# Performance work log

Hardware: AMD Instinct MI355X
Metric: run time of the kernel (lower is better)

## Reference

```python
import jax, jax.numpy as jnp
import numpy as np

B, LK, D, H = 16, 4096, 1024, 16
DK = D // H
EPS = 1e-5
NEG = -1.0e9


def _layernorm(x, g, b):
    m = jnp.mean(x, axis=-1, keepdims=True)
    v = jnp.mean((x - m) ** 2, axis=-1, keepdims=True)
    return (x - m) * jax.lax.rsqrt(v + EPS) * g + b


def setup_inputs() -> dict:
    key0 = jax.random.key(0)
    ks = jax.random.split(key0, 12)

    def lin(k, fan_in, fan_out):
        # torch nn.Linear default-ish scale; stored as [in, out] so y = x @ W + b
        return jax.random.normal(k, (fan_in, fan_out), jnp.float32) / np.float32(np.sqrt(fan_in))

    return {
        "query": jax.random.normal(ks[0], (B, 1, D), jnp.float32),
        "key": jax.random.normal(ks[1], (B, LK, D), jnp.float32),
        "mask": jax.random.randint(ks[2], (B, 1, LK), 0, 2, jnp.int32),
        "Wq": lin(ks[3], D, D), "bq": jnp.zeros((D,), jnp.float32),
        "Wk": lin(ks[4], D, D), "bk": jnp.zeros((D,), jnp.float32),
        "Wv": lin(ks[5], D, D), "bv": jnp.zeros((D,), jnp.float32),
        "Wo": lin(ks[6], D, D), "bo": jnp.zeros((D,), jnp.float32),
        "raw_thr": jnp.full((H, 1, 1), 0.1, jnp.float32),
        "Wvp": lin(ks[7], 2 * D, D),  # v_proj, no bias
        "W1": lin(ks[8], D, 2 * D), "b1": jnp.zeros((2 * D,), jnp.float32),
        "W2": lin(ks[9], 2 * D, D), "b2": jnp.zeros((D,), jnp.float32),
        "g1": jnp.ones((D,), jnp.float32), "be1": jnp.zeros((D,), jnp.float32),
        "g2": jnp.ones((D,), jnp.float32), "be2": jnp.zeros((D,), jnp.float32),
    }


def reference(query, key, mask, Wq, bq, Wk, bk, Wv, bv, Wo, bo, raw_thr,
              Wvp, W1, b1, W2, b2, g1, be1, g2, be2):
    b = query.shape[0]
    lk = key.shape[1]
    # v = cat(key, query.repeat(1, Lk, 1)) @ Wvp   (query has seq_len 1)
    v_in = jnp.concatenate([key, jnp.broadcast_to(query, (b, lk, D))], axis=2)
    v = v_in @ Wvp  # [B, Lk, D]

    Q = (query @ Wq + bq).reshape(b, 1, H, DK).transpose(0, 2, 1, 3)   # [B,H,1,DK]
    K = (key @ Wk + bk).reshape(b, lk, H, DK).transpose(0, 2, 1, 3)    # [B,H,Lk,DK]
    V = (v @ Wv + bv).reshape(b, lk, H, DK).transpose(0, 2, 1, 3)      # [B,H,Lk,DK]

    scores = jnp.einsum("bhqd,bhkd->bhqk", Q, K) / jnp.sqrt(jnp.float32(DK))
    # padding mask: [B,1,Lk] -> [B,1,1,Lk]
    scores = jnp.where(mask[:, None] == 0, NEG, scores)
    # learned per-head threshold: softplus(raw_thr) -> [1,H,1,1]
    thr = jax.nn.softplus(raw_thr)[None]
    scores = jnp.where(scores <= thr, NEG, scores)
    attn = jax.nn.softmax(scores, axis=-1)

    x = jnp.einsum("bhqk,bhkd->bhqd", attn, V)            # [B,H,1,DK]
    x = x.transpose(0, 2, 1, 3).reshape(b, 1, H * DK)      # [B,1,D]
    attn_out = x @ Wo + bo

    x = _layernorm(query + attn_out, g1, be1)
    ff = jax.nn.relu(x @ W1 + b1) @ W2 + b2
    x = _layernorm(x + ff, g2, be2)
    return x
```

## Files before the change

### kernel.cpp

```cpp
#include <hip/hip_runtime.h>
#include <hip/hip_bf16.h>

#define NB 16
#define NHD 16
#define ND 1024
#define NLK 4096
#define NFF 2048

typedef float f32x4 __attribute__((ext_vector_type(4)));
typedef float f32x2 __attribute__((ext_vector_type(2)));
typedef __bf16 bf16x2v __attribute__((ext_vector_type(2)));
typedef __bf16 bf16x4v __attribute__((ext_vector_type(4)));
typedef __bf16 bf16x8 __attribute__((ext_vector_type(8)));

__global__ void k_fill(float* out, int n, float v) {
  int i = blockIdx.x * 256 + threadIdx.x;
  if (i < n) out[i] = v;
}

__device__ __forceinline__ void gbar(unsigned* ctr, unsigned* flg, unsigned nblk) {
  __syncthreads();
  if (threadIdx.x == 0) {
    __hip_atomic_fetch_add(ctr, 1u, __ATOMIC_RELEASE, __HIP_MEMORY_SCOPE_AGENT);
    if (blockIdx.x == 0) {
      while (__hip_atomic_load(ctr, __ATOMIC_RELAXED, __HIP_MEMORY_SCOPE_AGENT) < nblk)
        __builtin_amdgcn_s_sleep(8);
      __hip_atomic_store(flg, 1u, __ATOMIC_RELEASE, __HIP_MEMORY_SCOPE_AGENT);
    } else {
      while (__hip_atomic_load(flg, __ATOMIC_RELAXED, __HIP_MEMORY_SCOPE_AGENT) == 0)
        __builtin_amdgcn_s_sleep(8);
    }
    __builtin_amdgcn_fence(__ATOMIC_ACQUIRE, "agent");
  }
  __syncthreads();
}

__global__ __launch_bounds__(256) void k_pre(const float* __restrict__ Wq,
                                             const float* __restrict__ bq,
                                             const float* __restrict__ Wvp,
                                             const float* __restrict__ query,
                                             const float* __restrict__ Wk,
                                             const float* __restrict__ bk,
                                             float* __restrict__ Qrow,
                                             float* __restrict__ cvec,
                                             __hip_bfloat16* __restrict__ wvpt,
                                             __hip_bfloat16* __restrict__ t_bf,
                                             float* __restrict__ s0,
                                             unsigned* __restrict__ bar) {
  __shared__ float pmem[9472];
  int blk = blockIdx.x;
  int t = threadIdx.x;
  if (blk < 128) {
    int which = blk >> 6;
    int jb = blk & 3;
    int i0 = ((blk >> 2) & 15) * 64;
    int j = jb * 256 + t;
    {
      int e = t * 4;
      int b = e >> 6, ii = e & 63;
      float4 v = *(const float4*)(query + (size_t)b * ND + i0 + ii);
      pmem[ii * 20 + b] = v.x;
      pmem[(ii + 1) * 20 + b] = v.y;
      pmem[(ii + 2) * 20 + b] = v.z;
      pmem[(ii + 3) * 20 + b] = v.w;
    }
    __syncthreads();
    float acc[16];
#pragma unroll
    for (int q = 0; q < 16; ++q) acc[q] = 0.f;
    for (int ii = 0; ii < 64; ++ii) {
      int i = i0 + ii;
      float wv = which ? Wvp[(size_t)(ND + i) * ND + j] : Wq[(size_t)i * ND + j];
      float qv[16];
      const float4* qp = (const float4*)&pmem[ii * 20];
      *(float4*)&qv[0] = qp[0];
      *(float4*)&qv[4] = qp[1];
      *(float4*)&qv[8] = qp[2];
      *(float4*)&qv[12] = qp[3];
#pragma unroll
      for (int q = 0; q < 16; ++q) acc[q] += wv * qv[q];
    }
    float* out = which ? cvec : Qrow;
    float bias = (!which && i0 == 0) ? bq[j] : 0.f;
#pragma unroll
    for (int q = 0; q < 16; ++q) atomicAdd(&out[q * ND + j], acc[q] + bias);
  } else {
    int tb = blk - 128;
    int n0 = (tb & 15) * 64;
    int k0base = (tb >> 4) * 256;
    for (int it = 0; it < 4; ++it) {
      int k0 = k0base + it * 64;
#pragma unroll
      for (int i = 0; i < 4; ++i) {
        int idx = t * 4 + i * 1024;
        int kk = idx >> 6, nn = idx & 63;
        float4 v = *(const float4*)(Wvp + (size_t)(k0 + kk) * ND + n0 + nn);
        pmem[kk * 68 + nn] = v.x;
        pmem[kk * 68 + nn + 1] = v.y;
        pmem[kk * 68 + nn + 2] = v.z;
        pmem[kk * 68 + nn + 3] = v.w;
      }
      __syncthreads();
#pragma unroll
      for (int i = 0; i < 4; ++i) {
        int idx = t * 4 + i * 1024;
        int nn = idx >> 6, kk = idx & 63;
        bf16x4v o;
#pragma unroll
        for (int j = 0; j < 4; ++j) o[j] = (__bf16)pmem[(kk + j) * 68 + nn];
        *(bf16x4v*)((__bf16*)wvpt + (size_t)(n0 + nn) * ND + k0 + kk) = o;
      }
      __syncthreads();
    }
  }
  gbar(&bar[5 * 32], &bar[256 + 5 * 32], 192);
  {
    int h = blk & 15, dblk = blk >> 4;
    float* qs = pmem;
    float* wks = pmem + 1024;
    if (blk < 128) {
      int lin = t * 4;
      int bb = lin >> 6, dk = lin & 63;
      *(float4*)&qs[bb * 64 + dk] = *(const float4*)(Qrow + bb * ND + h * 64 + dk);
#pragma unroll
      for (int e = 0; e < 8; ++e) {
        int l2 = e * 1024 + t * 4;
        int d = l2 >> 6, dk2 = l2 & 63;
        *(float4*)&wks[d * 66 + dk2] =
            *(const float4*)(Wk + (size_t)(dblk * 128 + d) * ND + h * 64 + dk2);
      }
    }
    __syncthreads();
    if (blk < 128) {
      if (dblk == 0 && t < 16) {
        float a = 0.f;
        const float* bkh = bk + h * 64;
        for (int jj = 0; jj < 64; ++jj) a += bkh[jj] * qs[t * 64 + jj];
        s0[t * 16 + h] = a;
      }
      int d = t >> 1, bh = (t & 1) * 8;
      float acc[8];
#pragma unroll
      for (int q = 0; q < 8; ++q) acc[q] = 0.f;
      for (int dk = 0; dk < 64; ++dk) {
        float wv = wks[d * 66 + dk];
#pragma unroll
        for (int q = 0; q < 8; ++q) acc[q] += wv * qs[(bh + q) * 64 + dk];
      }
#pragma unroll
      for (int q = 0; q < 8; ++q)
        t_bf[(size_t)((bh + q) * 16 + h) * ND + dblk * 128 + d] = (__hip_bfloat16)acc[q];
    }
  }
}

__global__ __launch_bounds__(512, 4) void k_flash(const float* __restrict__ key,
                                                  const __hip_bfloat16* __restrict__ t_bf,
                                                  const float* __restrict__ s0,
                                                  const float* __restrict__ raw_thr,
                                                  const int* __restrict__ mask,
                                                  __hip_bfloat16* __restrict__ pu,
                                                  float* __restrict__ mloc,
                                                  float* __restrict__ lloc) {
  int ch = blockIdx.x, b = blockIdx.y;
  int t = threadIdx.x;
  int wv = t >> 6, lane = t & 63, l15 = lane & 15, g4 = lane >> 4;
  __shared__ __align__(16) unsigned char lds_arena[79360];
  __bf16* kstage = (__bf16*)lds_arena;
  __bf16* psb = (__bf16*)(lds_arena + 65536);
  float* scr = (float*)(lds_arena + 74752);
  float* wls = (float*)(lds_arena + 76928);
  float* sm = (float*)(lds_arena + 78976);
  float* mrun = sm;
  float* lrun = sm + 16;
  float* fact = sm + 32;
  float* mnewv = sm + 48;
  float* thv = sm + 64;
  float* s0v = sm + 80;

  f32x2 pu_r[16];
#pragma unroll
  for (int h = 0; h < 16; ++h) pu_r[h] = (f32x2){0.f, 0.f};
  if (t < 16) {
    mrun[t] = -1.0e9f;
    lrun[t] = 0.f;
    thv[t] = log1pf(expf(raw_thr[t]));
    s0v[t] = s0[b * 16 + t];
  }
  __syncthreads();
  const float* keyb = key + (size_t)b * NLK * ND;
  const __hip_bfloat16* tb = t_bf + (size_t)(b * 16 + l15) * ND;
  int dsl = wv * 128;
  __bf16* kst_w = kstage + wv * 4096;
  int kk = t >> 4, hh = t & 15;
  int c16 = lane >> 2, bofs = (lane & 3) * 2;
  for (int sp = 0; sp < 4; ++sp) {
    int ks0 = ch * 128 + sp * 32;
    f32x4 sa0 = {0.f, 0.f, 0.f, 0.f}, sa1 = {0.f, 0.f, 0.f, 0.f};
#pragma unroll
    for (int st = 0; st < 4; ++st) {
      int d = dsl + st * 32 + g4 * 8;
      bf16x8 bfr = *(const bf16x8*)(tb + d);
      const float* a0p = keyb + (size_t)(ks0 + l15) * ND + d;
      const float* a1p = a0p + (size_t)16 * ND;
      float a0[8], a1[8];
      *(float4*)&a0[0] = *(const float4*)a0p;
      *(float4*)&a0[4] = *(const float4*)(a0p + 4);
      *(float4*)&a1[0] = *(const float4*)a1p;
      *(float4*)&a1[4] = *(const float4*)(a1p + 4);
      bf16x8 af0, af1;
#pragma unroll
      for (int j = 0; j < 8; ++j) {
        af0[j] = (__bf16)a0[j];
        af1[j] = (__bf16)a1[j];
      }
      int pos = (((st * 4 + g4) ^ l15) & 15) * 8;
      *(bf16x8*)(kst_w + l15 * 128 + pos) = af0;
      *(bf16x8*)(kst_w + (16 + l15) * 128 + pos) = af1;
      sa0 = __builtin_amdgcn_mfma_f32_16x16x32_bf16(af0, bfr, sa0, 0, 0, 0);
      sa1 = __builtin_amdgcn_mfma_f32_16x16x32_bf16(af1, bfr, sa1, 0, 0, 0);
    }
#pragma unroll
    for (int r = 0; r < 4; ++r) {
      psb[(wv * 32 + g4 * 4 + r) * 18 + l15] = (__bf16)sa0[r];
      psb[(wv * 32 + 16 + g4 * 4 + r) * 18 + l15] = (__bf16)sa1[r];
    }
    __syncthreads();
    float sum = 0.f;
#pragma unroll
    for (int w = 0; w < 8; ++w) sum += (float)psb[(w * 32 + kk) * 18 + hh];
    float sc_ = (sum + s0v[hh]) * 0.125f;
    int mv = mask[b * NLK + ks0 + kk];
    float sv = (mv != 0 && sc_ > thv[hh]) ? sc_ : -1.0e9f;
    scr[kk * 17 + hh] = sv;
    __syncthreads();
    if (wv == 0) {
      float m = -3.4e38f;
#pragma unroll
      for (int j = 0; j < 8; ++j) m = fmaxf(m, scr[(g4 * 8 + j) * 17 + l15]);
      m = fmaxf(m, __shfl_xor(m, 16, 64));
      m = fmaxf(m, __shfl_xor(m, 32, 64));
      if (lane < 16) {
        float mn = fmaxf(mrun[lane], m);
        mnewv[lane] = mn;
        fact[lane] = expf(mrun[lane] - mn);
        mrun[lane] = mn;
      }
    }
    __syncthreads();
    float w = expf(sv - mnewv[hh]);
    scr[kk * 17 + hh] = w;
    wls[kk * 16 + hh] = w;
    __syncthreads();
    if (wv == 0) {
      float s = 0.f;
#pragma unroll
      for (int j = 0; j < 8; ++j) s += scr[(g4 * 8 + j) * 17 + l15];
      s += __shfl_xor(s, 16, 64);
      s += __shfl_xor(s, 32, 64);
      if (lane < 16) lrun[lane] = lrun[lane] * fact[lane] + s;
    }
#pragma unroll
    for (int h = 0; h < 16; ++h) pu_r[h] *= fact[h];
    for (int k = 0; k < 32; ++k) {
      int phys = ((c16 ^ k) & 15) * 8;
      unsigned u = *(const unsigned*)(kst_w + k * 128 + phys + bofs);
      f32x2 kv;
      kv[0] = __uint_as_float(u << 16);
      kv[1] = __uint_as_float(u & 0xffff0000u);
      const f32x4* wr = (const f32x4*)&wls[k * 16];
      f32x4 w0 = wr[0], w1 = wr[1], w2 = wr[2], w3 = wr[3];
#pragma unroll
      for (int q = 0; q < 4; ++q) {
        pu_r[q] += w0[q] * kv;
        pu_r[4 + q] += w1[q] * kv;
        pu_r[8 + q] += w2[q] * kv;
        pu_r[12 + q] += w3[q] * kv;
      }
    }
  }
  int dlane = dsl + lane * 2;
  size_t pubase = (size_t)((b * 32 + ch) * 16) * ND + dlane;
#pragma unroll
  for (int h = 0; h < 16; ++h) {
    bf16x2v o;
    o[0] = (__bf16)pu_r[h][0];
    o[1] = (__bf16)pu_r[h][1];
    *(bf16x2v*)((__bf16*)pu + pubase + (size_t)h * ND) = o;
  }
  if (t < 16) {
    mloc[(b * 32 + ch) * 16 + t] = mrun[t];
    lloc[(b * 32 + ch) * 16 + t] = lrun[t];
  }
}

__global__ __launch_bounds__(256) void k_tail(
    const __hip_bfloat16* __restrict__ pu, const float* __restrict__ mloc,
    const float* __restrict__ lloc, __hip_bfloat16* __restrict__ u_bf,
    const __hip_bfloat16* __restrict__ wvpt,
    const float* __restrict__ cvec, const float* __restrict__ Wv,
    const float* __restrict__ bv, float* __restrict__ attn_x,
    const float* __restrict__ Wo, const float* __restrict__ bo,
    const float* __restrict__ query, float* __restrict__ r1,
    const float* __restrict__ g1, const float* __restrict__ be1,
    const float* __restrict__ W1, float* __restrict__ h1,
    const float* __restrict__ b1, const float* __restrict__ W2,
    float* __restrict__ out2, const float* __restrict__ b2,
    const float* __restrict__ g2, const float* __restrict__ be2,
    float* __restrict__ outp, unsigned* __restrict__ bar) {
  __shared__ float smf[2176];
  int blk = blockIdx.x, t = threadIdx.x;
  int wv = t >> 6, lane = t & 63, l15 = lane & 15, g4 = lane >> 4;

  {
    int g = blk * 256 + t;
    if (g < 16384) {
      attn_x[g] = 0.f;
      r1[g] = 0.f;
      out2[g] = 0.f;
    }
    if (g < 32768) h1[g] = 0.f;
    int b = blk >> 4, h = blk & 15;
    if (t < 32) {
      float m = mloc[(b * 32 + t) * 16 + h];
      float l = lloc[(b * 32 + t) * 16 + h];
      float mg = m;
      for (int o = 16; o > 0; o >>= 1) mg = fmaxf(mg, __shfl_xor(mg, o, 32));
      float term = l * expf(m - mg);
      float ls = term;
      for (int o = 16; o > 0; o >>= 1) ls += __shfl_xor(ls, o, 32);
      smf[t] = expf(m - mg) / ls;
    }
    __syncthreads();
    int d = t * 4;
    f32x4 acc = {0.f, 0.f, 0.f, 0.f};
    for (int c = 0; c < 32; ++c) {
      bf16x4v v4 = *(const bf16x4v*)((const __bf16*)pu +
                                     (size_t)((b * 32 + c) * 16 + h) * ND + d);
      f32x4 v = {(float)v4[0], (float)v4[1], (float)v4[2], (float)v4[3]};
      acc += smf[c] * v;
    }
    bf16x4v o;
#pragma unroll
    for (int j = 0; j < 4; ++j) o[j] = (__bf16)acc[j];
    *(bf16x4v*)((__bf16*)u_bf + (size_t)(b * 16 + h) * ND + d) = o;
  }
  gbar(&bar[0 * 32], &bar[256 + 0 * 32], 256);

  {
    int h = blk >> 4, d0 = (blk & 15) * 64;
    float* vb = smf;
    const __hip_bfloat16* ub = u_bf + (size_t)(l15 * 16 + h) * ND;
    const __hip_bfloat16* wb = wvpt + (size_t)(d0 + wv * 16 + l15) * ND;
    f32x4 acc = {0.f, 0.f, 0.f, 0.f};
    for (int ks = 0; ks < 32; ++ks) {
      int d = ks * 32 + g4 * 8;
      bf16x8 a = *(const bf16x8*)(ub + d);
      bf16x8 bb = *(const bf16x8*)(wb + d);
      acc = __builtin_amdgcn_mfma_f32_16x16x32_bf16(a, bb, acc, 0, 0, 0);
    }
#pragma unroll
    for (int r = 0; r < 4; ++r) {
      int b = g4 * 4 + r;
      int nn = wv * 16 + l15;
      vb[b * 68 + nn] = acc[r] + cvec[(size_t)b * ND + d0 + nn];
    }
    __syncthreads();
    int joff = t & 63, bg = t >> 6;
    int j = h * 64 + joff;
    float ax[4] = {0.f, 0.f, 0.f, 0.f};
    for (int dd = 0; dd < 64; ++dd) {
      float wv_ = Wv[(size_t)(d0 + dd) * ND + j];
#pragma unroll
      for (int q = 0; q < 4; ++q) ax[q] += wv_ * vb[(bg * 4 + q) * 68 + dd];
    }
#pragma unroll
    for (int q = 0; q < 4; ++q) {
      float val = ax[q];
      if ((blk & 15) == 0) val += bv[j];
      atomicAdd(&attn_x[(size_t)(bg * 4 + q) * ND + j], val);
    }
  }
  gbar(&bar[1 * 32], &bar[256 + 1 * 32], 256);

  if (blk < 128) {
    int j0 = (blk & 7) * 128;
    int d0 = (blk >> 3) * 64;
    float* ax = smf;
    {
      int lin = t * 4;
      int bb = lin >> 6, dd = lin & 63;
      *(float4*)&ax[bb * 68 + dd] = *(const float4*)(attn_x + (size_t)bb * ND + d0 + dd);
    }
    __syncthreads();
    int joff = t & 127, bg = t >> 7;
    int j = j0 + joff;
    float acc[8];
#pragma unroll
    for (int q = 0; q < 8; ++q) acc[q] = 0.f;
    for (int dd = 0; dd < 64; ++dd) {
      float wv_ = Wo[(size_t)(d0 + dd) * ND + j];
#pragma unroll
      for (int q = 0; q < 8; ++q) acc[q] += wv_ * ax[(bg * 8 + q) * 68 + dd];
    }
#pragma unroll
    for (int q = 0; q < 8; ++q) {
      int bb = bg * 8 + q;
      float val = acc[q];
      if ((blk >> 3) == 0) val += bo[j] + query[(size_t)bb * ND + j];
      atomicAdd(&r1[(size_t)bb * ND + j], val);
    }
  } else {
    __syncthreads();
  }
  gbar(&bar[2 * 32], &bar[256 + 2 * 32], 256);

  if (blk < 128) {
    int n = (blk & 7) * 256 + t;
    int d0 = (blk >> 3) * 64;
    float* xs = smf;
    float* mv_s = smf + 1984;
    float* iv_s = smf + 2000;
    {
      int row = t >> 4, seg = t & 15;
      float s = 0.f, s2 = 0.f;
      const float* rp = r1 + (size_t)row * ND + seg * 64;
      for (int q = 0; q < 16; ++q) {
        float4 v = *(const float4*)(rp + q * 4);
        s += v.x + v.y + v.z + v.w;
        s2 += v.x * v.x + v.y * v.y + v.z * v.z + v.w * v.w;
      }
      for (int o = 1; o < 16; o <<= 1) {
        s += __shfl_xor(s, o, 16);
        s2 += __shfl_xor(s2, o, 16);
      }
      if (seg == 0) {
        float mean = s * (1.f / ND);
        float var = s2 * (1.f / ND) - mean * mean;
        mv_s[row] = mean;
        iv_s[row] = rsqrtf(var + 1e-5f);
      }
    }
    __syncthreads();
    {
      int e = t * 4;
      int bb = e >> 6, dd = e & 63;
      float4 v = *(const float4*)(r1 + (size_t)bb * ND + d0 + dd);
      float4 g = *(const float4*)(g1 + d0 + dd);
      float4 be = *(const float4*)(be1 + d0 + dd);
      float m = mv_s[bb], iv = iv_s[bb];
      xs[bb * 68 + dd] = (v.x - m) * iv * g.x + be.x;
      xs[bb * 68 + dd + 1] = (v.y - m) * iv * g.y + be.y;
      xs[bb * 68 + dd + 2] = (v.z - m) * iv * g.z + be.z;
      xs[bb * 68 + dd + 3] = (v.w - m) * iv * g.w + be.w;
    }
    __syncthreads();
    float acc[16];
#pragma unroll
    for (int q = 0; q < 16; ++q) acc[q] = 0.f;
    for (int dd = 0; dd < 64; ++dd) {
      float wv_ = W1[(size_t)(d0 + dd) * NFF + n];
#pragma unroll
      for (int q = 0; q < 16; ++q) acc[q] += wv_ * xs[q * 68 + dd];
    }
#pragma unroll
    for (int q = 0; q < 16; ++q) atomicAdd(&h1[(size_t)q * NFF + n], acc[q]);
  } else {
    __syncthreads();
    __syncthreads();
  }
  gbar(&bar[3 * 32], &bar[256 + 3 * 32], 256);

  if (blk < 128) {
    int j0 = (blk & 7) * 128;
    int n0 = (blk >> 3) * 128;
    float* hs = smf;
#pragma unroll
    for (int e = 0; e < 8; ++e) {
      int lin = e * 256 + t;
      int bb = lin >> 7, nn = lin & 127;
      float hv = h1[(size_t)bb * NFF + n0 + nn] + b1[n0 + nn];
      hs[bb * 132 + nn] = fmaxf(hv, 0.f);
    }
    __syncthreads();
    int joff = t & 127, bg = t >> 7;
    int j = j0 + joff;
    float acc[8];
#pragma unroll
    for (int q = 0; q < 8; ++q) acc[q] = 0.f;
    for (int nn = 0; nn < 128; ++nn) {
      float wv_ = W2[(size_t)(n0 + nn) * ND + j];
#pragma unroll
      for (int q = 0; q < 8; ++q) acc[q] += wv_ * hs[(bg * 8 + q) * 132 + nn];
    }
#pragma unroll
    for (int q = 0; q < 8; ++q) atomicAdd(&out2[(size_t)(bg * 8 + q) * ND + j], acc[q]);
  } else {
    __syncthreads();
  }
  gbar(&bar[4 * 32], &bar[256 + 4 * 32], 256);

  if (blk < 16) {
    int b = blk;
    float* rs = smf;
    float* rs2 = smf + 256;
    float4 v = *(const float4*)(r1 + (size_t)b * ND + t * 4);
    float s = v.x + v.y + v.z + v.w;
    float s2 = v.x * v.x + v.y * v.y + v.z * v.z + v.w * v.w;
    rs[t] = s;
    rs2[t] = s2;
    __syncthreads();
    for (int st = 128; st > 0; st >>= 1) {
      if (t < st) {
        rs[t] += rs[t + st];
        rs2[t] += rs2[t + st];
      }
      __syncthreads();
    }
    float mean = rs[0] * (1.f / ND);
    float var = rs2[0] * (1.f / ND) - mean * mean;
    float inv = rsqrtf(var + 1e-5f);
    float4 g = *(const float4*)(g1 + t * 4);
    float4 be = *(const float4*)(be1 + t * 4);
    float4 o2 = *(const float4*)(out2 + (size_t)b * ND + t * 4);
    float4 bb2 = *(const float4*)(b2 + t * 4);
    float4 v2;
    v2.x = (v.x - mean) * inv * g.x + be.x + o2.x + bb2.x;
    v2.y = (v.y - mean) * inv * g.y + be.y + o2.y + bb2.y;
    v2.z = (v.z - mean) * inv * g.z + be.z + o2.z + bb2.z;
    v2.w = (v.w - mean) * inv * g.w + be.w + o2.w + bb2.w;
    __syncthreads();
    s = v2.x + v2.y + v2.z + v2.w;
    s2 = v2.x * v2.x + v2.y * v2.y + v2.z * v2.z + v2.w * v2.w;
    rs[t] = s;
    rs2[t] = s2;
    __syncthreads();
    for (int st = 128; st > 0; st >>= 1) {
      if (t < st) {
        rs[t] += rs[t + st];
        rs2[t] += rs2[t + st];
      }
      __syncthreads();
    }
    float mean2 = rs[0] * (1.f / ND);
    float var2 = rs2[0] * (1.f / ND) - mean2 * mean2;
    float inv2 = rsqrtf(var2 + 1e-5f);
    float4 gg = *(const float4*)(g2 + t * 4);
    float4 bbe = *(const float4*)(be2 + t * 4);
    float4 o;
    o.x = (v2.x - mean2) * inv2 * gg.x + bbe.x;
    o.y = (v2.y - mean2) * inv2 * gg.y + bbe.y;
    o.z = (v2.z - mean2) * inv2 * gg.z + bbe.z;
    o.w = (v2.w - mean2) * inv2 * gg.w + bbe.w;
    *(float4*)(outp + (size_t)b * ND + t * 4) = o;
  }
}

extern "C" void kernel_launch(void* const* d_in, const int* in_sizes, int n_in,
                              void* d_out, int out_size, void* d_ws, size_t ws_size,
                              hipStream_t stream) {
  const float* query = (const float*)d_in[0];
  const float* key = (const float*)d_in[1];
  const int* mask = (const int*)d_in[2];
  const float* Wq = (const float*)d_in[3];
  const float* bq = (const float*)d_in[4];
  const float* Wk = (const float*)d_in[5];
  const float* bk = (const float*)d_in[6];
  const float* Wv = (const float*)d_in[7];
  const float* bv = (const float*)d_in[8];
  const float* Wo = (const float*)d_in[9];
  const float* bo = (const float*)d_in[10];
  const float* raw_thr = (const float*)d_in[11];
  const float* Wvp = (const float*)d_in[12];
  const float* W1 = (const float*)d_in[13];
  const float* b1 = (const float*)d_in[14];
  const float* W2 = (const float*)d_in[15];
  const float* b2 = (const float*)d_in[16];
  const float* g1 = (const float*)d_in[17];
  const float* be1 = (const float*)d_in[18];
  const float* g2 = (const float*)d_in[19];
  const float* be2 = (const float*)d_in[20];

  const size_t OFF_QROW = 0;
  const size_t OFF_C = 65536;
  const size_t OFF_BAR = 131072;
  const size_t ZERO_BYTES = 135168;
  const size_t OFF_ATTNX = 135168;
  const size_t OFF_R1 = 200704;
  const size_t OFF_H1 = 266240;
  const size_t OFF_OUT2 = 397312;
  const size_t OFF_S0 = 462848;
  const size_t OFF_MLOC = 463872;
  const size_t OFF_LLOC = 496640;
  const size_t OFF_TBF = 529408;
  const size_t OFF_UBF = 1053696;
  const size_t OFF_WVPT = 1577984;
  const size_t OFF_PU = 4723712;
  const size_t TOTAL = 21500928;

  if (ws_size < TOTAL) {
    k_fill<<<dim3((out_size + 255) / 256), dim3(256), 0, stream>>>((float*)d_out, out_size,
                                                                   12345.0f);
    return;
  }

  char* wsb = (char*)d_ws;
  float* Qrow = (float*)(wsb + OFF_QROW);
  float* cvec = (float*)(wsb + OFF_C);
  unsigned* bar = (unsigned*)(wsb + OFF_BAR);
  float* attn_x = (float*)(wsb + OFF_ATTNX);
  float* r1 = (float*)(wsb + OFF_R1);
  float* h1 = (float*)(wsb + OFF_H1);
  float* out2 = (float*)(wsb + OFF_OUT2);
  float* s0 = (float*)(wsb + OFF_S0);
  float* mloc = (float*)(wsb + OFF_MLOC);
  float* lloc = (float*)(wsb + OFF_LLOC);
  __hip_bfloat16* t_bf = (__hip_bfloat16*)(wsb + OFF_TBF);
  __hip_bfloat16* u_bf = (__hip_bfloat16*)(wsb + OFF_UBF);
  __hip_bfloat16* wvpt = (__hip_bfloat16*)(wsb + OFF_WVPT);
  __hip_bfloat16* pu = (__hip_bfloat16*)(wsb + OFF_PU);

  hipMemsetAsync(d_ws, 0, ZERO_BYTES, stream);

  k_pre<<<dim3(192), dim3(256), 0, stream>>>(Wq, bq, Wvp, query, Wk, bk, Qrow, cvec, wvpt,
                                             t_bf, s0, bar);
  k_flash<<<dim3(32, 16), dim3(512), 0, stream>>>(key, t_bf, s0, raw_thr, mask, pu, mloc, lloc);
  k_tail<<<dim3(256), dim3(256), 0, stream>>>(pu, mloc, lloc, u_bf, wvpt, cvec, Wv, bv,
                                              attn_x, Wo, bo, query, r1, g1, be1, W1, h1, b1,
                                              W2, out2, b2, g2, be2, (float*)d_out, bar);
}
```

Measured before the change: 205.4 us.

## Fuse pre, flash and tail kernels into one persistent megakernel with grid barriers

New measurement: 418.3 us. +103.7%, slower.

```diff
diff --git a/kernel.cpp b/kernel.cpp
--- a/kernel.cpp
+++ b/kernel.cpp
@@ -18,7 +18,9 @@
   if (i < n) out[i] = v;
 }
 
-__device__ __forceinline__ void gbar(unsigned* ctr, unsigned* flg, unsigned nblk) {
+__device__ __forceinline__ void gbar(unsigned* bar, int slot, unsigned nblk) {
+  unsigned* ctr = &bar[slot * 32];
+  unsigned* flg = &bar[512 + slot * 32];
   __syncthreads();
   if (threadIdx.x == 0) {
     __hip_atomic_fetch_add(ctr, 1u, __ATOMIC_RELEASE, __HIP_MEMORY_SCOPE_AGENT);
@@ -35,323 +37,317 @@
   __syncthreads();
 }
 
-__global__ __launch_bounds__(256) void k_pre(const float* __restrict__ Wq,
-                                             const float* __restrict__ bq,
-                                             const float* __restrict__ Wvp,
-                                             const float* __restrict__ query,
-                                             const float* __restrict__ Wk,
-                                             const float* __restrict__ bk,
-                                             float* __restrict__ Qrow,
-                                             float* __restrict__ cvec,
-                                             __hip_bfloat16* __restrict__ wvpt,
-                                             __hip_bfloat16* __restrict__ t_bf,
-                                             float* __restrict__ s0,
-                                             unsigned* __restrict__ bar) {
-  __shared__ float pmem[9472];
-  int blk = blockIdx.x;
-  int t = threadIdx.x;
+__global__ __launch_bounds__(512, 4) void k_mega(
+    const float* __restrict__ query, const float* __restrict__ key,
+    const int* __restrict__ mask, const float* __restrict__ Wq,
+    const float* __restrict__ bq, const float* __restrict__ Wk,
+    const float* __restrict__ bk, const float* __restrict__ Wv,
+    const float* __restrict__ bv, const float* __restrict__ Wo,
+    const float* __restrict__ bo, const float* __restrict__ raw_thr,
+    const float* __restrict__ Wvp, const float* __restrict__ W1,
+    const float* __restrict__ b1, const float* __restrict__ W2,
+    const float* __restrict__ b2, const float* __restrict__ g1,
+    const float* __restrict__ be1, const float* __restrict__ g2,
+    const float* __restrict__ be2,
+    float* __restrict__ Qrow, float* __restrict__ cvec, float* __restrict__ attn_x,
+    float* __restrict__ r1, float* __restrict__ h1, float* __restrict__ out2,
+    float* __restrict__ s0, float* __restrict__ mloc, float* __restrict__ lloc,
+    __hip_bfloat16* __restrict__ t_bf, __hip_bfloat16* __restrict__ u_bf,
+    __hip_bfloat16* __restrict__ wvpt, __hip_bfloat16* __restrict__ pu,
+    float* __restrict__ outp, unsigned* __restrict__ bar) {
+  __shared__ __align__(16) unsigned char arena[79360];
+  float* af = (float*)arena;
+  int blk = blockIdx.x, t = threadIdx.x;
+  int wv = t >> 6, lane = t & 63, l15 = lane & 15, g4 = lane >> 4;
+  int half = t >> 8, vt = t & 255;
+
+  {
+    int g = blk * 512 + t;
+    if (g < 16384) {
+      Qrow[g] = 0.f;
+      cvec[g] = 0.f;
+      attn_x[g] = 0.f;
+      r1[g] = 0.f;
+      out2[g] = 0.f;
+    }
+    if (g < 32768) h1[g] = 0.f;
+  }
+  gbar(bar, 0, 512);
+
   if (blk < 128) {
     int which = blk >> 6;
-    int jb = blk & 3;
-    int i0 = ((blk >> 2) & 15) * 64;
-    int j = jb * 256 + t;
-    {
+    int jb = (blk >> 5) & 1;
+    int i0c = blk & 31;
+    int i0 = i0c * 32;
+    int j = jb * 512 + t;
+    if (t < 128) {
       int e = t * 4;
-      int b = e >> 6, ii = e & 63;
+      int b = e >> 5, ii = e & 31;
       float4 v = *(const float4*)(query + (size_t)b * ND + i0 + ii);
-      pmem[ii * 20 + b] = v.x;
-      pmem[(ii + 1) * 20 + b] = v.y;
-      pmem[(ii + 2) * 20 + b] = v.z;
-      pmem[(ii + 3) * 20 + b] = v.w;
+      af[ii * 20 + b] = v.x;
+      af[(ii + 1) * 20 + b] = v.y;
+      af[(ii + 2) * 20 + b] = v.z;
+      af[(ii + 3) * 20 + b] = v.w;
     }
     __syncthreads();
     float acc[16];
 #pragma unroll
     for (int q = 0; q < 16; ++q) acc[q] = 0.f;
-    for (int ii = 0; ii < 64; ++ii) {
+    for (int ii = 0; ii < 32; ++ii) {
       int i = i0 + ii;
-      float wv = which ? Wvp[(size_t)(ND + i) * ND + j] : Wq[(size_t)i * ND + j];
+      float wvv = which ? Wvp[(size_t)(ND + i) * ND + j] : Wq[(size_t)i * ND + j];
       float qv[16];
-      const float4* qp = (const float4*)&pmem[ii * 20];
+      const float4* qp = (const float4*)&af[ii * 20];
       *(float4*)&qv[0] = qp[0];
       *(float4*)&qv[4] = qp[1];
       *(float4*)&qv[8] = qp[2];
       *(float4*)&qv[12] = qp[3];
 #pragma unroll
-      for (int q = 0; q < 16; ++q) acc[q] += wv * qv[q];
+      for (int q = 0; q < 16; ++q) acc[q] += wvv * qv[q];
     }
     float* out = which ? cvec : Qrow;
-    float bias = (!which && i0 == 0) ? bq[j] : 0.f;
+    float bias = (!which && i0c == 0) ? bq[j] : 0.f;
 #pragma unroll
     for (int q = 0; q < 16; ++q) atomicAdd(&out[q * ND + j], acc[q] + bias);
-  } else {
+  } else if (blk < 192) {
     int tb = blk - 128;
     int n0 = (tb & 15) * 64;
     int k0base = (tb >> 4) * 256;
     for (int it = 0; it < 4; ++it) {
       int k0 = k0base + it * 64;
 #pragma unroll
-      for (int i = 0; i < 4; ++i) {
-        int idx = t * 4 + i * 1024;
+      for (int i = 0; i < 2; ++i) {
+        int idx = t * 4 + i * 2048;
         int kk = idx >> 6, nn = idx & 63;
         float4 v = *(const float4*)(Wvp + (size_t)(k0 + kk) * ND + n0 + nn);
-        pmem[kk * 68 + nn] = v.x;
-        pmem[kk * 68 + nn + 1] = v.y;
-        pmem[kk * 68 + nn + 2] = v.z;
-        pmem[kk * 68 + nn + 3] = v.w;
-      }
-      __syncthreads();
-#pragma unroll
-      for (int i = 0; i < 4; ++i) {
-        int idx = t * 4 + i * 1024;
+        af[kk * 68 + nn] = v.x;
+        af[kk * 68 + nn + 1] = v.y;
+        af[kk * 68 + nn + 2] = v.z;
+        af[kk * 68 + nn + 3] = v.w;
+      }
+      __syncthreads();
+#pragma unroll
+      for (int i = 0; i < 2; ++i) {
+        int idx = t * 4 + i * 2048;
         int nn = idx >> 6, kk = idx & 63;
         bf16x4v o;
 #pragma unroll
-        for (int j = 0; j < 4; ++j) o[j] = (__bf16)pmem[(kk + j) * 68 + nn];
+        for (int jj = 0; jj < 4; ++jj) o[jj] = (__bf16)af[(kk + jj) * 68 + nn];
         *(bf16x4v*)((__bf16*)wvpt + (size_t)(n0 + nn) * ND + k0 + kk) = o;
       }
       __syncthreads();
     }
   }
-  gbar(&bar[5 * 32], &bar[256 + 5 * 32], 192);
-  {
-    int h = blk & 15, dblk = blk >> 4;
-    float* qs = pmem;
-    float* wks = pmem + 1024;
-    if (blk < 128) {
-      int lin = t * 4;
+  gbar(bar, 1, 512);
+
+  if (blk < 64) {
+    int h = blk & 15;
+    int dblk = (blk >> 4) * 2 + half;
+    float* pm = af + half * 9472;
+    float* qs = pm;
+    float* wks = pm + 1024;
+    {
+      int lin = vt * 4;
       int bb = lin >> 6, dk = lin & 63;
       *(float4*)&qs[bb * 64 + dk] = *(const float4*)(Qrow + bb * ND + h * 64 + dk);
-#pragma unroll
-      for (int e = 0; e < 8; ++e) {
-        int l2 = e * 1024 + t * 4;
-        int d = l2 >> 6, dk2 = l2 & 63;
-        *(float4*)&wks[d * 66 + dk2] =
-            *(const float4*)(Wk + (size_t)(dblk * 128 + d) * ND + h * 64 + dk2);
-      }
-    }
-    __syncthreads();
-    if (blk < 128) {
-      if (dblk == 0 && t < 16) {
-        float a = 0.f;
-        const float* bkh = bk + h * 64;
-        for (int jj = 0; jj < 64; ++jj) a += bkh[jj] * qs[t * 64 + jj];
-        s0[t * 16 + h] = a;
-      }
-      int d = t >> 1, bh = (t & 1) * 8;
-      float acc[8];
-#pragma unroll
-      for (int q = 0; q < 8; ++q) acc[q] = 0.f;
-      for (int dk = 0; dk < 64; ++dk) {
-        float wv = wks[d * 66 + dk];
-#pragma unroll
-        for (int q = 0; q < 8; ++q) acc[q] += wv * qs[(bh + q) * 64 + dk];
-      }
-#pragma unroll
-      for (int q = 0; q < 8; ++q)
-        t_bf[(size_t)((bh + q) * 16 + h) * ND + dblk * 128 + d] = (__hip_bfloat16)acc[q];
-    }
-  }
-}
-
-__global__ __launch_bounds__(512, 4) void k_flash(const float* __restrict__ key,
-                                                  const __hip_bfloat16* __restrict__ t_bf,
-                                                  const float* __restrict__ s0,
-                                                  const float* __restrict__ raw_thr,
-                                                  const int* __restrict__ mask,
-                                                  __hip_bfloat16* __restrict__ pu,
-                                                  float* __restrict__ mloc,
-                                                  float* __restrict__ lloc) {
-  int ch = blockIdx.x, b = blockIdx.y;
-  int t = threadIdx.x;
-  int wv = t >> 6, lane = t & 63, l15 = lane & 15, g4 = lane >> 4;
-  __shared__ __align__(16) unsigned char lds_arena[79360];
-  __bf16* kstage = (__bf16*)lds_arena;
-  __bf16* psb = (__bf16*)(lds_arena + 65536);
-  float* scr = (float*)(lds_arena + 74752);
-  float* wls = (float*)(lds_arena + 76928);
-  float* sm = (float*)(lds_arena + 78976);
-  float* mrun = sm;
-  float* lrun = sm + 16;
-  float* fact = sm + 32;
-  float* mnewv = sm + 48;
-  float* thv = sm + 64;
-  float* s0v = sm + 80;
-
-  f32x2 pu_r[16];
-#pragma unroll
-  for (int h = 0; h < 16; ++h) pu_r[h] = (f32x2){0.f, 0.f};
-  if (t < 16) {
-    mrun[t] = -1.0e9f;
-    lrun[t] = 0.f;
-    thv[t] = log1pf(expf(raw_thr[t]));
-    s0v[t] = s0[b * 16 + t];
-  }
-  __syncthreads();
-  const float* keyb = key + (size_t)b * NLK * ND;
-  const __hip_bfloat16* tb = t_bf + (size_t)(b * 16 + l15) * ND;
-  int dsl = wv * 128;
-  __bf16* kst_w = kstage + wv * 4096;
-  int kk = t >> 4, hh = t & 15;
-  int c16 = lane >> 2, bofs = (lane & 3) * 2;
-  for (int sp = 0; sp < 4; ++sp) {
-    int ks0 = ch * 128 + sp * 32;
-    f32x4 sa0 = {0.f, 0.f, 0.f, 0.f}, sa1 = {0.f, 0.f, 0.f, 0.f};
-#pragma unroll
-    for (int st = 0; st < 4; ++st) {
-      int d = dsl + st * 32 + g4 * 8;
-      bf16x8 bfr = *(const bf16x8*)(tb + d);
-      const float* a0p = keyb + (size_t)(ks0 + l15) * ND + d;
-      const float* a1p = a0p + (size_t)16 * ND;
-      float a0[8], a1[8];
-      *(float4*)&a0[0] = *(const float4*)a0p;
-      *(float4*)&a0[4] = *(const float4*)(a0p + 4);
-      *(float4*)&a1[0] = *(const float4*)a1p;
-      *(float4*)&a1[4] = *(const float4*)(a1p + 4);
-      bf16x8 af0, af1;
-#pragma unroll
-      for (int j = 0; j < 8; ++j) {
-        af0[j] = (__bf16)a0[j];
-        af1[j] = (__bf16)a1[j];
-      }
-      int pos = (((st * 4 + g4) ^ l15) & 15) * 8;
-      *(bf16x8*)(kst_w + l15 * 128 + pos) = af0;
-      *(bf16x8*)(kst_w + (16 + l15) * 128 + pos) = af1;
-      sa0 = __builtin_amdgcn_mfma_f32_16x16x32_bf16(af0, bfr, sa0, 0, 0, 0);
-      sa1 = __builtin_amdgcn_mfma_f32_16x16x32_bf16(af1, bfr, sa1, 0, 0, 0);
-    }
-#pragma unroll
-    for (int r = 0; r < 4; ++r) {
-      psb[(wv * 32 + g4 * 4 + r) * 18 + l15] = (__bf16)sa0[r];
-      psb[(wv * 32 + 16 + g4 * 4 + r) * 18 + l15] = (__bf16)sa1[r];
-    }
-    __syncthreads();
-    float sum = 0.f;
-#pragma unroll
-    for (int w = 0; w < 8; ++w) sum += (float)psb[(w * 32 + kk) * 18 + hh];
-    float sc_ = (sum + s0v[hh]) * 0.125f;
-    int mv = mask[b * NLK + ks0 + kk];
-    float sv = (mv != 0 && sc_ > thv[hh]) ? sc_ : -1.0e9f;
-    scr[kk * 17 + hh] = sv;
-    __syncthreads();
-    if (wv == 0) {
-      float m = -3.4e38f;
-#pragma unroll
-      for (int j = 0; j < 8; ++j) m = fmaxf(m, scr[(g4 * 8 + j) * 17 + l15]);
-      m = fmaxf(m, __shfl_xor(m, 16, 64));
-      m = fmaxf(m, __shfl_xor(m, 32, 64));
-      if (lane < 16) {
-        float mn = fmaxf(mrun[lane], m);
-        mnewv[lane] = mn;
-        fact[lane] = expf(mrun[lane] - mn);
-        mrun[lane] = mn;
-      }
-    }
-    __syncthreads();
-    float w = expf(sv - mnewv[hh]);
-    scr[kk * 17 + hh] = w;
-    wls[kk * 16 + hh] = w;
-    __syncthreads();
-    if (wv == 0) {
-      float s = 0.f;
-#pragma unroll
-      for (int j = 0; j < 8; ++j) s += scr[(g4 * 8 + j) * 17 + l15];
-      s += __shfl_xor(s, 16, 64);
-      s += __shfl_xor(s, 32, 64);
-      if (lane < 16) lrun[lane] = lrun[lane] * fact[lane] + s;
-    }
-#pragma unroll
-    for (int h = 0; h < 16; ++h) pu_r[h] *= fact[h];
-    for (int k = 0; k < 32; ++k) {
-      int phys = ((c16 ^ k) & 15) * 8;
-      unsigned u = *(const unsigned*)(kst_w + k * 128 + phys + bofs);
-      f32x2 kv;
-      kv[0] = __uint_as_float(u << 16);
-      kv[1] = __uint_as_float(u & 0xffff0000u);
-      const f32x4* wr = (const f32x4*)&wls[k * 16];
-      f32x4 w0 = wr[0], w1 = wr[1], w2 = wr[2], w3 = wr[3];
-#pragma unroll
-      for (int q = 0; q < 4; ++q) {
-        pu_r[q] += w0[q] * kv;
-        pu_r[4 + q] += w1[q] * kv;
-        pu_r[8 + q] += w2[q] * kv;
-        pu_r[12 + q] += w3[q] * kv;
-      }
-    }
-  }
-  int dlane = dsl + lane * 2;
-  size_t pubase = (size_t)((b * 32 + ch) * 16) * ND + dlane;
-#pragma unroll
-  for (int h = 0; h < 16; ++h) {
-    bf16x2v o;
-    o[0] = (__bf16)pu_r[h][0];
-    o[1] = (__bf16)pu_r[h][1];
-    *(bf16x2v*)((__bf16*)pu + pubase + (size_t)h * ND) = o;
-  }
-  if (t < 16) {
-    mloc[(b * 32 + ch) * 16 + t] = mrun[t];
-    lloc[(b * 32 + ch) * 16 + t] = lrun[t];
-  }
-}
-
-__global__ __launch_bounds__(256) void k_tail(
-    const __hip_bfloat16* __restrict__ pu, const float* __restrict__ mloc,
-    const float* __restrict__ lloc, __hip_bfloat16* __restrict__ u_bf,
-    const __hip_bfloat16* __restrict__ wvpt,
-    const float* __restrict__ cvec, const float* __restrict__ Wv,
-    const float* __restrict__ bv, float* __restrict__ attn_x,
-    const float* __restrict__ Wo, const float* __restrict__ bo,
-    const float* __restrict__ query, float* __restrict__ r1,
-    const float* __restrict__ g1, const float* __restrict__ be1,
-    const float* __restrict__ W1, float* __restrict__ h1,
-    const float* __restrict__ b1, const float* __restrict__ W2,
-    float* __restrict__ out2, const float* __restrict__ b2,
-    const float* __restrict__ g2, const float* __restrict__ be2,
-    float* __restrict__ outp, unsigned* __restrict__ bar) {
-  __shared__ float smf[2176];
-  int blk = blockIdx.x, t = threadIdx.x;
-  int wv = t >> 6, lane = t & 63, l15 = lane & 15, g4 = lane >> 4;
+    }
+#pragma unroll
+    for (int e = 0; e < 8; ++e) {
+      int l2 = e * 1024 + vt * 4;
+      int d = l2 >> 6, dk2 = l2 & 63;
+      *(float4*)&wks[d * 66 + dk2] =
+          *(const float4*)(Wk + (size_t)(dblk * 128 + d) * ND + h * 64 + dk2);
+    }
+    __syncthreads();
+    if (dblk == 0 && vt < 16) {
+      float a = 0.f;
+      const float* bkh = bk + h * 64;
+      for (int jj = 0; jj < 64; ++jj) a += bkh[jj] * qs[vt * 64 + jj];
+      s0[vt * 16 + h] = a;
+    }
+    int d = vt >> 1, bh = (vt & 1) * 8;
+    float acc[8];
+#pragma unroll
+    for (int q = 0; q < 8; ++q) acc[q] = 0.f;
+    for (int dk = 0; dk < 64; ++dk) {
+      float wvv = wks[d * 66 + dk];
+#pragma unroll
+      for (int q = 0; q < 8; ++q) acc[q] += wvv * qs[(bh + q) * 64 + dk];
+    }
+#pragma unroll
+    for (int q = 0; q < 8; ++q)
+      t_bf[(size_t)((bh + q) * 16 + h) * ND + dblk * 128 + d] = (__hip_bfloat16)acc[q];
+  }
+  gbar(bar, 2, 512);
 
   {
-    int g = blk * 256 + t;
-    if (g < 16384) {
-      attn_x[g] = 0.f;
-      r1[g] = 0.f;
-      out2[g] = 0.f;
-    }
-    if (g < 32768) h1[g] = 0.f;
-    int b = blk >> 4, h = blk & 15;
-    if (t < 32) {
-      float m = mloc[(b * 32 + t) * 16 + h];
-      float l = lloc[(b * 32 + t) * 16 + h];
+    int ch = blk & 31, b = blk >> 5;
+    __bf16* kstage = (__bf16*)arena;
+    __bf16* psb = (__bf16*)(arena + 65536);
+    float* scr = (float*)(arena + 74752);
+    float* wls = (float*)(arena + 76928);
+    float* sm = (float*)(arena + 78976);
+    float* mrun = sm;
+    float* lrun = sm + 16;
+    float* fact = sm + 32;
+    float* mnewv = sm + 48;
+    float* thv = sm + 64;
+    float* s0v = sm + 80;
+
+    f32x2 pu_r[16];
+#pragma unroll
+    for (int h = 0; h < 16; ++h) pu_r[h] = (f32x2){0.f, 0.f};
+    if (t < 16) {
+      mrun[t] = -1.0e9f;
+      lrun[t] = 0.f;
+      thv[t] = log1pf(expf(raw_thr[t]));
+      s0v[t] = s0[b * 16 + t];
+    }
+    __syncthreads();
+    const float* keyb = key + (size_t)b * NLK * ND;
+    const __hip_bfloat16* tb = t_bf + (size_t)(b * 16 + l15) * ND;
+    int dsl = wv * 128;
+    __bf16* kst_w = kstage + wv * 4096;
+    int kk = t >> 4, hh = t & 15;
+    int c16 = lane >> 2, bofs = (lane & 3) * 2;
+    for (int sp = 0; sp < 4; ++sp) {
+      int ks0 = ch * 128 + sp * 32;
+      f32x4 sa0 = {0.f, 0.f, 0.f, 0.f}, sa1 = {0.f, 0.f, 0.f, 0.f};
+#pragma unroll
+      for (int st = 0; st < 4; ++st) {
+        int d = dsl + st * 32 + g4 * 8;
+        bf16x8 bfr = *(const bf16x8*)(tb + d);
+        const float* a0p = keyb + (size_t)(ks0 + l15) * ND + d;
+        const float* a1p = a0p + (size_t)16 * ND;
+        float a0[8], a1[8];
+        *(float4*)&a0[0] = *(const float4*)a0p;
+        *(float4*)&a0[4] = *(const float4*)(a0p + 4);
+        *(float4*)&a1[0] = *(const float4*)a1p;
+        *(float4*)&a1[4] = *(const float4*)(a1p + 4);
+        bf16x8 af0, af1;
+#pragma unroll
+        for (int j = 0; j < 8; ++j) {
+          af0[j] = (__bf16)a0[j];
+          af1[j] = (__bf16)a1[j];
+        }
+        int pos = (((st * 4 + g4) ^ l15) & 15) * 8;
+        *(bf16x8*)(kst_w + l15 * 128 + pos) = af0;
+        *(bf16x8*)(kst_w + (16 + l15) * 128 + pos) = af1;
+        sa0 = __builtin_amdgcn_mfma_f32_16x16x32_bf16(af0, bfr, sa0, 0, 0, 0);
+        sa1 = __builtin_amdgcn_mfma_f32_16x16x32_bf16(af1, bfr, sa1, 0, 0, 0);
+      }
+#pragma unroll
+      for (int r = 0; r < 4; ++r) {
+        psb[(wv * 32 + g4 * 4 + r) * 18 + l15] = (__bf16)sa0[r];
+        psb[(wv * 32 + 16 + g4 * 4 + r) * 18 + l15] = (__bf16)sa1[r];
+      }
+      __syncthreads();
+      float sum = 0.f;
+#pragma unroll
+      for (int w = 0; w < 8; ++w) sum += (float)psb[(w * 32 + kk) * 18 + hh];
+      float sc_ = (sum + s0v[hh]) * 0.125f;
+      int mv = mask[b * NLK + ks0 + kk];
+      float sv = (mv != 0 && sc_ > thv[hh]) ? sc_ : -1.0e9f;
+      scr[kk * 17 + hh] = sv;
+      __syncthreads();
+      if (wv == 0) {
+        float m = -3.4e38f;
+#pragma unroll
+        for (int j = 0; j < 8; ++j) m = fmaxf(m, scr[(g4 * 8 + j) * 17 + l15]);
+        m = fmaxf(m, __shfl_xor(m, 16, 64));
+        m = fmaxf(m, __shfl_xor(m, 32, 64));
+        if (lane < 16) {
+          float mn = fmaxf(mrun[lane], m);
+          mnewv[lane] = mn;
+          fact[lane] = expf(mrun[lane] - mn);
+          mrun[lane] = mn;
+        }
+      }
+      __syncthreads();
+      float w = expf(sv - mnewv[hh]);
+      scr[kk * 17 + hh] = w;
+      wls[kk * 16 + hh] = w;
+      __syncthreads();
+      if (wv == 0) {
+        float s = 0.f;
+#pragma unroll
+        for (int j = 0; j < 8; ++j) s += scr[(g4 * 8 + j) * 17 + l15];
+        s += __shfl_xor(s, 16, 64);
+        s += __shfl_xor(s, 32, 64);
+        if (lane < 16) lrun[lane] = lrun[lane] * fact[lane] + s;
+      }
+#pragma unroll
+      for (int h = 0; h < 16; ++h) pu_r[h] *= fact[h];
+      for (int k = 0; k < 32; ++k) {
+        int phys = ((c16 ^ k) & 15) * 8;
+        unsigned u = *(const unsigned*)(kst_w + k * 128 + phys + bofs);
+        f32x2 kv;
+        kv[0] = __uint_as_float(u << 16);
+        kv[1] = __uint_as_float(u & 0xffff0000u);
+        const f32x4* wr = (const f32x4*)&wls[k * 16];
+        f32x4 w0 = wr[0], w1 = wr[1], w2 = wr[2], w3 = wr[3];
+#pragma unroll
+        for (int q = 0; q < 4; ++q) {
+          pu_r[q] += w0[q] * kv;
+          pu_r[4 + q] += w1[q] * kv;
+          pu_r[8 + q] += w2[q] * kv;
+          pu_r[12 + q] += w3[q] * kv;
+        }
+      }
+    }
+    int dlane = dsl + lane * 2;
+    size_t pubase = (size_t)((b * 32 + ch) * 16) * ND + dlane;
+#pragma unroll
+    for (int h = 0; h < 16; ++h) {
+      bf16x2v o;
+      o[0] = (__bf16)pu_r[h][0];
+      o[1] = (__bf16)pu_r[h][1];
+      *(bf16x2v*)((__bf16*)pu + pubase + (size_t)h * ND) = o;
+    }
+    if (t < 16) {
+      mloc[(b * 32 + ch) * 16 + t] = mrun[t];
+      lloc[(b * 32 + ch) * 16 + t] = lrun[t];
+    }
+  }
+  gbar(bar, 3, 512);
+
+  if (blk < 128) {
+    int unit = blk * 2 + half;
+    int b = unit >> 4, h = unit & 15;
+    float* sc = af + half * 32;
+    if (vt < 32) {
+      float m = mloc[(b * 32 + vt) * 16 + h];
+      float l = lloc[(b * 32 + vt) * 16 + h];
       float mg = m;
       for (int o = 16; o > 0; o >>= 1) mg = fmaxf(mg, __shfl_xor(mg, o, 32));
       float term = l * expf(m - mg);
       float ls = term;
       for (int o = 16; o > 0; o >>= 1) ls += __shfl_xor(ls, o, 32);
-      smf[t] = expf(m - mg) / ls;
-    }
-    __syncthreads();
-    int d = t * 4;
+      sc[vt] = expf(m - mg) / ls;
+    }
+    __syncthreads();
+    int d = vt * 4;
     f32x4 acc = {0.f, 0.f, 0.f, 0.f};
     for (int c = 0; c < 32; ++c) {
       bf16x4v v4 = *(const bf16x4v*)((const __bf16*)pu +
                                      (size_t)((b * 32 + c) * 16 + h) * ND + d);
       f32x4 v = {(float)v4[0], (float)v4[1], (float)v4[2], (float)v4[3]};
-      acc += smf[c] * v;
+      acc += sc[c] * v;
     }
     bf16x4v o;
 #pragma unroll
     for (int j = 0; j < 4; ++j) o[j] = (__bf16)acc[j];
     *(bf16x4v*)((__bf16*)u_bf + (size_t)(b * 16 + h) * ND + d) = o;
   }
-  gbar(&bar[0 * 32], &bar[256 + 0 * 32], 256);
-
-  {
-    int h = blk >> 4, d0 = (blk & 15) * 64;
-    float* vb = smf;
+  gbar(bar, 4, 512);
+
+  if (blk < 128) {
+    int uu = blk * 2 + half;
+    int h = uu >> 4, d0 = (uu & 15) * 64;
+    int wv2 = wv & 3;
+    float* vb = af + half * 1088;
     const __hip_bfloat16* ub = u_bf + (size_t)(l15 * 16 + h) * ND;
-    const __hip_bfloat16* wb = wvpt + (size_t)(d0 + wv * 16 + l15) * ND;
+    const __hip_bfloat16* wb = wvpt + (size_t)(d0 + wv2 * 16 + l15) * ND;
     f32x4 acc = {0.f, 0.f, 0.f, 0.f};
     for (int ks = 0; ks < 32; ++ks) {
       int d = ks * 32 + g4 * 8;
@@ -362,11 +358,11 @@
 #pragma unroll
     for (int r = 0; r < 4; ++r) {
       int b = g4 * 4 + r;
-      int nn = wv * 16 + l15;
+      int nn = wv2 * 16 + l15;
       vb[b * 68 + nn] = acc[r] + cvec[(size_t)b * ND + d0 + nn];
     }
     __syncthreads();
-    int joff = t & 63, bg = t >> 6;
+    int joff = vt & 63, bg = vt >> 6;
     int j = h * 64 + joff;
     float ax[4] = {0.f, 0.f, 0.f, 0.f};
     for (int dd = 0; dd < 64; ++dd) {
@@ -377,23 +373,24 @@
 #pragma unroll
     for (int q = 0; q < 4; ++q) {
       float val = ax[q];
-      if ((blk & 15) == 0) val += bv[j];
+      if ((uu & 15) == 0) val += bv[j];
       atomicAdd(&attn_x[(size_t)(bg * 4 + q) * ND + j], val);
     }
   }
-  gbar(&bar[1 * 32], &bar[256 + 1 * 32], 256);
-
-  if (blk < 128) {
-    int j0 = (blk & 7) * 128;
-    int d0 = (blk >> 3) * 64;
-    float* ax = smf;
+  gbar(bar, 5, 512);
+
+  if (blk < 64) {
+    int unit = blk * 2 + half;
+    int j0 = (unit & 7) * 128;
+    int d0 = (unit >> 3) * 64;
+    float* ax = af + half * 1088;
     {
-      int lin = t * 4;
+      int lin = vt * 4;
       int bb = lin >> 6, dd = lin & 63;
       *(float4*)&ax[bb * 68 + dd] = *(const float4*)(attn_x + (size_t)bb * ND + d0 + dd);
     }
     __syncthreads();
-    int joff = t & 127, bg = t >> 7;
+    int joff = vt & 127, bg = vt >> 7;
     int j = j0 + joff;
     float acc[8];
 #pragma unroll
@@ -407,22 +404,22 @@
     for (int q = 0; q < 8; ++q) {
       int bb = bg * 8 + q;
       float val = acc[q];
-      if ((blk >> 3) == 0) val += bo[j] + query[(size_t)bb * ND + j];
+      if ((unit >> 3) == 0) val += bo[j] + query[(size_t)bb * ND + j];
       atomicAdd(&r1[(size_t)bb * ND + j], val);
     }
-  } else {
-    __syncthreads();
-  }
-  gbar(&bar[2 * 32], &bar[256 + 2 * 32], 256);
-
-  if (blk < 128) {
-    int n = (blk & 7) * 256 + t;
-    int d0 = (blk >> 3) * 64;
-    float* xs = smf;
-    float* mv_s = smf + 1984;
-    float* iv_s = smf + 2000;
+  }
+  gbar(bar, 6, 512);
+
+  if (blk < 64) {
+    int unit = blk * 2 + half;
+    int n = (unit & 7) * 256 + vt;
+    int d0 = (unit >> 3) * 64;
+    float* base = af + half * 2048;
+    float* xs = base;
+    float* mv_s = base + 1984;
+    float* iv_s = base + 2000;
     {
-      int row = t >> 4, seg = t & 15;
+      int row = vt >> 4, seg = vt & 15;
       float s = 0.f, s2 = 0.f;
       const float* rp = r1 + (size_t)row * ND + seg * 64;
       for (int q = 0; q < 16; ++q) {
@@ -443,7 +440,7 @@
     }
     __syncthreads();
     {
-      int e = t * 4;
+      int e = vt * 4;
       int bb = e >> 6, dd = e & 63;
       float4 v = *(const float4*)(r1 + (size_t)bb * ND + d0 + dd);
       float4 g = *(const float4*)(g1 + d0 + dd);
@@ -465,25 +462,23 @@
     }
 #pragma unroll
     for (int q = 0; q < 16; ++q) atomicAdd(&h1[(size_t)q * NFF + n], acc[q]);
-  } else {
-    __syncthreads();
-    __syncthreads();
-  }
-  gbar(&bar[3 * 32], &bar[256 + 3 * 32], 256);
-
-  if (blk < 128) {
-    int j0 = (blk & 7) * 128;
-    int n0 = (blk >> 3) * 128;
-    float* hs = smf;
+  }
+  gbar(bar, 7, 512);
+
+  if (blk < 64) {
+    int unit = blk * 2 + half;
+    int j0 = (unit & 7) * 128;
+    int n0 = (unit >> 3) * 128;
+    float* hs = af + half * 2112;
 #pragma unroll
     for (int e = 0; e < 8; ++e) {
-      int lin = e * 256 + t;
+      int lin = e * 256 + vt;
       int bb = lin >> 7, nn = lin & 127;
       float hv = h1[(size_t)bb * NFF + n0 + nn] + b1[n0 + nn];
       hs[bb * 132 + nn] = fmaxf(hv, 0.f);
     }
     __syncthreads();
-    int joff = t & 127, bg = t >> 7;
+    int joff = vt & 127, bg = vt >> 7;
     int j = j0 + joff;
     float acc[8];
 #pragma unroll
@@ -495,35 +490,34 @@
     }
 #pragma unroll
     for (int q = 0; q < 8; ++q) atomicAdd(&out2[(size_t)(bg * 8 + q) * ND + j], acc[q]);
-  } else {
-    __syncthreads();
-  }
-  gbar(&bar[4 * 32], &bar[256 + 4 * 32], 256);
-
-  if (blk < 16) {
-    int b = blk;
-    float* rs = smf;
-    float* rs2 = smf + 256;
-    float4 v = *(const float4*)(r1 + (size_t)b * ND + t * 4);
+  }
+  gbar(bar, 8, 512);
+
+  if (blk < 8) {
+    int b = blk * 2 + half;
+    float* base = af + half * 1024;
+    float* rs = base;
+    float* rs2 = base + 256;
+    float4 v = *(const float4*)(r1 + (size_t)b * ND + vt * 4);
     float s = v.x + v.y + v.z + v.w;
     float s2 = v.x * v.x + v.y * v.y + v.z * v.z + v.w * v.w;
-    rs[t] = s;
-    rs2[t] = s2;
+    rs[vt] = s;
+    rs2[vt] = s2;
     __syncthreads();
     for (int st = 128; st > 0; st >>= 1) {
-      if (t < st) {
-        rs[t] += rs[t + st];
-        rs2[t] += rs2[t + st];
+      if (vt < st) {
+        rs[vt] += rs[vt + st];
+        rs2[vt] += rs2[vt + st];
       }
       __syncthreads();
     }
     float mean = rs[0] * (1.f / ND);
     float var = rs2[0] * (1.f / ND) - mean * mean;
     float inv = rsqrtf(var + 1e-5f);
-    float4 g = *(const float4*)(g1 + t * 4);
-    float4 be = *(const float4*)(be1 + t * 4);
-    float4 o2 = *(const float4*)(out2 + (size_t)b * ND + t * 4);
-    float4 bb2 = *(const float4*)(b2 + t * 4);
+    float4 g = *(const float4*)(g1 + vt * 4);
+    float4 be = *(const float4*)(be1 + vt * 4);
+    float4 o2 = *(const float4*)(out2 + (size_t)b * ND + vt * 4);
+    float4 bb2 = *(const float4*)(b2 + vt * 4);
     float4 v2;
     v2.x = (v.x - mean) * inv * g.x + be.x + o2.x + bb2.x;
     v2.y = (v.y - mean) * inv * g.y + be.y + o2.y + bb2.y;
@@ -532,27 +526,27 @@
     __syncthreads();
     s = v2.x + v2.y + v2.z + v2.w;
     s2 = v2.x * v2.x + v2.y * v2.y + v2.z * v2.z + v2.w * v2.w;
-    rs[t] = s;
-    rs2[t] = s2;
+    rs[vt] = s;
+    rs2[vt] = s2;
     __syncthreads();
     for (int st = 128; st > 0; st >>= 1) {
-      if (t < st) {
-        rs[t] += rs[t + st];
-        rs2[t] += rs2[t + st];
+      if (vt < st) {
+        rs[vt] += rs[vt + st];
+        rs2[vt] += rs2[vt + st];
       }
       __syncthreads();
     }
     float mean2 = rs[0] * (1.f / ND);
     float var2 = rs2[0] * (1.f / ND) - mean2 * mean2;
     float inv2 = rsqrtf(var2 + 1e-5f);
-    float4 gg = *(const float4*)(g2 + t * 4);
-    float4 bbe = *(const float4*)(be2 + t * 4);
+    float4 gg = *(const float4*)(g2 + vt * 4);
+    float4 bbe = *(const float4*)(be2 + vt * 4);
     float4 o;
     o.x = (v2.x - mean2) * inv2 * gg.x + bbe.x;
     o.y = (v2.y - mean2) * inv2 * gg.y + bbe.y;
     o.z = (v2.z - mean2) * inv2 * gg.z + bbe.z;
     o.w = (v2.w - mean2) * inv2 * gg.w + bbe.w;
-    *(float4*)(outp + (size_t)b * ND + t * 4) = o;
+    *(float4*)(outp + (size_t)b * ND + vt * 4) = o;
   }
 }
 
@@ -581,10 +575,10 @@
   const float* g2 = (const float*)d_in[19];
   const float* be2 = (const float*)d_in[20];
 
-  const size_t OFF_QROW = 0;
-  const size_t OFF_C = 65536;
-  const size_t OFF_BAR = 131072;
-  const size_t ZERO_BYTES = 135168;
+  const size_t OFF_BAR = 0;
+  const size_t ZERO_BYTES = 4096;
+  const size_t OFF_QROW = 4096;
+  const size_t OFF_C = 69632;
   const size_t OFF_ATTNX = 135168;
   const size_t OFF_R1 = 200704;
   const size_t OFF_H1 = 266240;
@@ -595,8 +589,8 @@
   const size_t OFF_TBF = 529408;
   const size_t OFF_UBF = 1053696;
   const size_t OFF_WVPT = 1577984;
-  const size_t OFF_PU = 4723712;
-  const size_t TOTAL = 21500928;
+  const size_t OFF_PU = 3675136;
+  const size_t TOTAL = 20452352;
 
   if (ws_size < TOTAL) {
     k_fill<<<dim3((out_size + 255) / 256), dim3(256), 0, stream>>>((float*)d_out, out_size,
@@ -605,9 +599,9 @@
   }
 
   char* wsb = (char*)d_ws;
+  unsigned* bar = (unsigned*)(wsb + OFF_BAR);
   float* Qrow = (float*)(wsb + OFF_QROW);
   float* cvec = (float*)(wsb + OFF_C);
-  unsigned* bar = (unsigned*)(wsb + OFF_BAR);
   float* attn_x = (float*)(wsb + OFF_ATTNX);
   float* r1 = (float*)(wsb + OFF_R1);
   float* h1 = (float*)(wsb + OFF_H1);
@@ -622,10 +616,8 @@
 
   hipMemsetAsync(d_ws, 0, ZERO_BYTES, stream);
 
-  k_pre<<<dim3(192), dim3(256), 0, stream>>>(Wq, bq, Wvp, query, Wk, bk, Qrow, cvec, wvpt,
-                                             t_bf, s0, bar);
-  k_flash<<<dim3(32, 16), dim3(512), 0, stream>>>(key, t_bf, s0, raw_thr, mask, pu, mloc, lloc);
-  k_tail<<<dim3(256), dim3(256), 0, stream>>>(pu, mloc, lloc, u_bf, wvpt, cvec, Wv, bv,
-                                              attn_x, Wo, bo, query, r1, g1, be1, W1, h1, b1,
-                                              W2, out2, b2, g2, be2, (float*)d_out, bar);
+  k_mega<<<dim3(512), dim3(512), 0, stream>>>(
+      query, key, mask, Wq, bq, Wk, bk, Wv, bv, Wo, bo, raw_thr, Wvp, W1, b1, W2, b2,
+      g1, be1, g2, be2, Qrow, cvec, attn_x, r1, h1, out2, s0, mloc, lloc, t_bf, u_bf,
+      wvpt, pu, (float*)d_out, bar);
 }
```
